# Performance work log

Measured on AMD Instinct MI355X. Metric: run time of the kernel, lower is better.

The kernel has to match this reference:

```python
import jax, jax.numpy as jnp
import numpy as np

N = 20000      # nodes
E = 320000     # edges (before self-loops)
IN = 128       # in_features
H = 8          # heads
C = 120        # out channels per head
SLOPE = 0.2    # LeakyReLU negative slope (PyG default)


def setup_inputs() -> dict:
    key = jax.random.key(0)
    k = jax.random.split(key, 8)
    x = jax.random.normal(k[0], (N, IN), jnp.float32)
    edge_index = jax.random.randint(k[1], (2, E), 0, N)  # [2,E], row0=src, row1=dst
    W = jax.random.normal(k[2], (IN, H * C), jnp.float32) / np.sqrt(IN)
    att_src = jax.random.normal(k[3], (H, C), jnp.float32) * 0.1
    att_dst = jax.random.normal(k[4], (H, C), jnp.float32) * 0.1
    bias = jnp.zeros((H * C,), jnp.float32)
    fc_w = jax.random.normal(k[5], (H * C, 2), jnp.float32) / np.sqrt(H * C)
    fc_b = jnp.zeros((2,), jnp.float32)
    return dict(x=x, edge_index=edge_index, W=W, att_src=att_src,
                att_dst=att_dst, bias=bias, fc_w=fc_w, fc_b=fc_b)


def reference(x, edge_index, W, att_src, att_dst, bias, fc_w, fc_b):
    n = x.shape[0]
    # add self loops (GATConv default add_self_loops=True)
    loops = jnp.arange(n, dtype=edge_index.dtype)
    ei = jnp.concatenate([edge_index, jnp.stack([loops, loops])], axis=1)
    src, dst = ei[0], ei[1]
    # per-head linear projection: [n, H, C]
    xp = (x @ W).reshape(n, H, C)
    # per-node attention logits
    a_s = jnp.einsum('nhc,hc->nh', xp, att_src)  # [n,H]
    a_d = jnp.einsum('nhc,hc->nh', xp, att_dst)  # [n,H]
    # edge-wise logits + LeakyReLU: [Etot,H]
    e = jax.nn.leaky_relu(a_s[src] + a_d[dst], SLOPE)
    # segment softmax over incoming edges of each destination node
    emax = jax.lax.stop_gradient(jax.ops.segment_max(e, dst, num_segments=n))
    ee = jnp.exp(e - emax[dst])
    denom = jax.ops.segment_sum(ee, dst, num_segments=n)
    alpha = ee / denom[dst]                      # [Etot,H]
    # scatter-aggregate weighted messages: [n,H,C]
    out = jax.ops.segment_sum(alpha[:, :, None] * xp[src], dst, num_segments=n)
    out = out.reshape(n, H * C) + bias           # concat heads + bias
    return out @ fc_w + fc_b                     # final Linear -> [n,2]
```

## Files before the change

kernel.cpp:

```cpp
#include <hip/hip_runtime.h>

#define NN    20000
#define EDGES 320000
#define HH    8
#define CC    120
#define HC    960
#define SLOPE 0.2f
#define BUCKET 64
#define NB    64
#define CH    (EDGES / NB)
#define NPAIR (NN / 2)


__global__ __launch_bounds__(256) void prep_kernel(const float* __restrict__ W,
                                                   const float* __restrict__ att_src,
                                                   const float* __restrict__ att_dst,
                                                   const float* __restrict__ bias,
                                                   const float* __restrict__ fc_w,
                                                   const float* __restrict__ fc_b,
                                                   const int* __restrict__ ei,
                                                   float* __restrict__ U,
                                                   float* __restrict__ cbias,
                                                   unsigned* __restrict__ hist,
                                                   unsigned* __restrict__ rank) {
  __shared__ unsigned hsh[NPAIR];
  int t = threadIdx.x, b = blockIdx.x;
  int l = t & 63;
  if (b < 256) {
    int p = b * 4 + (t >> 6);
    int k = p >> 3, h = p & 7;
    const float* wrow = W + (size_t)k * HC + h * CC;
    const float* asv  = att_src + h * CC;
    const float* adv  = att_dst + h * CC;
    const float2* fv  = (const float2*)fc_w + h * CC;
    bool tail = (l < CC - 64);
    float w0 = wrow[l],            w1 = tail ? wrow[64 + l] : 0.f;
    float s0 = asv[l],             s1 = tail ? asv[64 + l] : 0.f;
    float d0 = adv[l],             d1 = tail ? adv[64 + l] : 0.f;
    float2 f0 = fv[l];
    float2 f1 = tail ? fv[64 + l] : make_float2(0.f, 0.f);
    float a_s = w0 * s0 + w1 * s1;
    float a_d = w0 * d0 + w1 * d1;
    float z0  = w0 * f0.x + w1 * f1.x;
    float z1  = w0 * f0.y + w1 * f1.y;
#pragma unroll
    for (int m = 1; m < 64; m <<= 1) {
      a_s += __shfl_xor(a_s, m);
      a_d += __shfl_xor(a_d, m);
      z0  += __shfl_xor(z0, m);
      z1  += __shfl_xor(z1, m);
    }
    if (l == 0) {
      float* u = U + k * 32 + 4 * h;
      u[0] = a_s; u[1] = z0; u[2] = z1; u[3] = a_d;
    }
  } else if (b == 256) {
    if (t < 128) {
      int j = t >> 6;
      float acc = 0.f;
      for (int m = l; m < HC; m += 64) acc = fmaf(bias[m], fc_w[m * 2 + j], acc);
#pragma unroll
      for (int m = 1; m < 64; m <<= 1) acc += __shfl_xor(acc, m);
      if (l == 0) cbias[j] = acc + fc_b[j];
    }
  } else {
    int c = b - 257;
    for (int i = t; i < NPAIR; i += 256) hsh[i] = 0u;
    __syncthreads();
    const int* dsts = ei + EDGES + c * CH;
    unsigned* rnk = rank + c * CH;
    for (int i = t; i < CH; i += 256) {
      int d = dsts[i];
      unsigned old = atomicAdd(&hsh[d >> 1], (d & 1) ? (1u << 16) : 1u);
      rnk[i] = (d & 1) ? (old >> 16) : (old & 0xFFFFu);
    }
    __syncthreads();
    unsigned* hrow = hist + (size_t)c * NPAIR;
    for (int i = t; i < NPAIR; i += 256) hrow[i] = hsh[i];
  }
}

__global__ __launch_bounds__(256) void scan_kernel(const unsigned* __restrict__ hist,
                                                   unsigned* __restrict__ base,
                                                   unsigned* __restrict__ deg) {
  int j = blockIdx.x * 256 + threadIdx.x;
  if (j >= NPAIR) return;
  unsigned sA = 0, sB = 0;
#pragma unroll 8
  for (int c = 0; c < NB; ++c) {
    unsigned v = hist[(size_t)c * NPAIR + j];
    base[(size_t)c * NPAIR + j] = sA | (sB << 16);
    sA += v & 0xFFFFu;
    sB += v >> 16;
  }
  deg[2 * j]     = sA;
  deg[2 * j + 1] = sB;
}

#define XSTR 132
__global__ __launch_bounds__(128) void projplace_kernel(const float* __restrict__ x,
                                                        const float* __restrict__ U,
                                                        const int* __restrict__ ei,
                                                        const unsigned* __restrict__ base,
                                                        const unsigned* __restrict__ rank,
                                                        unsigned* __restrict__ list,
                                                        float* __restrict__ P) {
  int t = threadIdx.x;
  int b = blockIdx.x;

  if (b >= 625) {
    int e0 = (b - 625) * 256 + t;
#pragma unroll
    for (int j = 0; j < 2; ++j) {
      int e = e0 + j * 128;
      int d = ei[EDGES + e];
      unsigned r = rank[e];
      unsigned c = (unsigned)e / (unsigned)CH;
      unsigned packed = base[(size_t)c * NPAIR + (d >> 1)];
      unsigned bs = (d & 1) ? (packed >> 16) : (packed & 0xFFFFu);
      list[(size_t)d * BUCKET + bs + r] = (unsigned)ei[e];
    }
    return;
  }

  __shared__ float xs[32 * XSTR];
  __shared__ float Us[128 * 32];
  int n0 = b * 32;
  const float4* xg = (const float4*)(x + (size_t)n0 * 128);
  const float4* U4 = (const float4*)U;
  float4 xv[8], uv[8];
#pragma unroll
  for (int j = 0; j < 8; ++j) xv[j] = xg[t + j * 128];
#pragma unroll
  for (int j = 0; j < 8; ++j) uv[j] = U4[t + j * 128];
#pragma unroll
  for (int j = 0; j < 8; ++j) {
    int i = t + j * 128;
    *(float4*)(xs + (i >> 5) * XSTR + (i & 31) * 4) = xv[j];
    ((float4*)Us)[i] = uv[j];
  }
  __syncthreads();

  int rq = t >> 3, cq = t & 7;
  float a00 = 0.f, a01 = 0.f, a02 = 0.f, a03 = 0.f;
  float a10 = 0.f, a11 = 0.f, a12 = 0.f, a13 = 0.f;
  const float* xr0 = xs + rq * XSTR;
  const float* xr1 = xs + (rq + 16) * XSTR;
#pragma unroll 4
  for (int k4 = 0; k4 < 32; ++k4) {
    float4 xa = *(const float4*)(xr0 + k4 * 4);
    float4 xb = *(const float4*)(xr1 + k4 * 4);
    float4 u0 = *(const float4*)(Us + (k4 * 4 + 0) * 32 + 4 * cq);
    float4 u1 = *(const float4*)(Us + (k4 * 4 + 1) * 32 + 4 * cq);
    float4 u2 = *(const float4*)(Us + (k4 * 4 + 2) * 32 + 4 * cq);
    float4 u3 = *(const float4*)(Us + (k4 * 4 + 3) * 32 + 4 * cq);
    a00 = fmaf(xa.x, u0.x, a00); a01 = fmaf(xa.x, u0.y, a01);
    a02 = fmaf(xa.x, u0.z, a02); a03 = fmaf(xa.x, u0.w, a03);
    a10 = fmaf(xb.x, u0.x, a10); a11 = fmaf(xb.x, u0.y, a11);
    a12 = fmaf(xb.x, u0.z, a12); a13 = fmaf(xb.x, u0.w, a13);
    a00 = fmaf(xa.y, u1.x, a00); a01 = fmaf(xa.y, u1.y, a01);
    a02 = fmaf(xa.y, u1.z, a02); a03 = fmaf(xa.y, u1.w, a03);
    a10 = fmaf(xb.y, u1.x, a10); a11 = fmaf(xb.y, u1.y, a11);
    a12 = fmaf(xb.y, u1.z, a12); a13 = fmaf(xb.y, u1.w, a13);
    a00 = fmaf(xa.z, u2.x, a00); a01 = fmaf(xa.z, u2.y, a01);
    a02 = fmaf(xa.z, u2.z, a02); a03 = fmaf(xa.z, u2.w, a03);
    a10 = fmaf(xb.z, u2.x, a10); a11 = fmaf(xb.z, u2.y, a11);
    a12 = fmaf(xb.z, u2.z, a12); a13 = fmaf(xb.z, u2.w, a13);
    a00 = fmaf(xa.w, u3.x, a00); a01 = fmaf(xa.w, u3.y, a01);
    a02 = fmaf(xa.w, u3.z, a02); a03 = fmaf(xa.w, u3.w, a03);
    a10 = fmaf(xb.w, u3.x, a10); a11 = fmaf(xb.w, u3.y, a11);
    a12 = fmaf(xb.w, u3.z, a12); a13 = fmaf(xb.w, u3.w, a13);
  }
  *(float4*)(P + (size_t)(n0 + rq) * 32 + 4 * cq) =
      make_float4(a00, a01, a02, a03);
  *(float4*)(P + (size_t)(n0 + rq + 16) * 32 + 4 * cq) =
      make_float4(a10, a11, a12, a13);
}

__global__ __launch_bounds__(256) void gather_kernel(const unsigned* __restrict__ deg_,
                                                     const unsigned* __restrict__ list,
                                                     const float* __restrict__ P,
                                                     const float* __restrict__ cbias,
                                                     float* __restrict__ out) {
  int t = threadIdx.x;
  int wave = t >> 6;
  int lane = t & 63;
  int h = lane & 7;
  int o = lane >> 3;
  int dst = blockIdx.x * 4 + wave;

  const float* pd = P + (size_t)dst * 32;
  float4 pd4 = *(const float4*)(pd + 4 * h);
  float ad = pd4.w;
  unsigned deg = deg_[dst];
  unsigned rv = list[(size_t)dst * BUCKET + lane];

  float accd = 0.f, acc0 = 0.f, acc1 = 0.f;
  if (o == 0) {
    float v = pd4.x + ad;
    v = (v > 0.f) ? v : SLOPE * v;
    float ex = __expf(v);
    accd = ex;
    acc0 = ex * pd4.y;
    acc1 = ex * pd4.z;
  }

  unsigned e0 = o, e1 = o + 8, e2 = o + 16, e3 = o + 24;
  unsigned s0 = __shfl(rv, (int)e0);
  unsigned s1 = __shfl(rv, (int)e1);
  unsigned s2 = __shfl(rv, (int)e2);
  unsigned s3 = __shfl(rv, (int)e3);
  bool m0 = e0 < deg, m1 = e1 < deg, m2 = e2 < deg, m3 = e3 < deg;
  unsigned a0 = m0 ? s0 : (unsigned)dst;
  unsigned a1 = m1 ? s1 : (unsigned)dst;
  unsigned a2 = m2 ? s2 : (unsigned)dst;
  unsigned a3 = m3 ? s3 : (unsigned)dst;
  float4 q0 = *(const float4*)(P + (size_t)a0 * 32 + 4 * h);
  float4 q1 = *(const float4*)(P + (size_t)a1 * 32 + 4 * h);
  float4 q2 = *(const float4*)(P + (size_t)a2 * 32 + 4 * h);
  float4 q3 = *(const float4*)(P + (size_t)a3 * 32 + 4 * h);
  if (m0) {
    float v = q0.x + ad; v = (v > 0.f) ? v : SLOPE * v;
    float ex = __expf(v);
    accd += ex; acc0 = fmaf(ex, q0.y, acc0); acc1 = fmaf(ex, q0.z, acc1);
  }
  if (m1) {
    float v = q1.x + ad; v = (v > 0.f) ? v : SLOPE * v;
    float ex = __expf(v);
    accd += ex; acc0 = fmaf(ex, q1.y, acc0); acc1 = fmaf(ex, q1.z, acc1);
  }
  if (m2) {
    float v = q2.x + ad; v = (v > 0.f) ? v : SLOPE * v;
    float ex = __expf(v);
    accd += ex; acc0 = fmaf(ex, q2.y, acc0); acc1 = fmaf(ex, q2.z, acc1);
  }
  if (m3) {
    float v = q3.x + ad; v = (v > 0.f) ? v : SLOPE * v;
    float ex = __expf(v);
    accd += ex; acc0 = fmaf(ex, q3.y, acc0); acc1 = fmaf(ex, q3.z, acc1);
  }
  if (deg > 32u) {
    unsigned iters = (deg - 32u + 7u) >> 3;
    unsigned e = 32u + (unsigned)o;
    for (unsigned i = 0; i < iters; ++i, e += 8u) {
      unsigned src = __shfl(rv, (int)e);
      if (e < deg) {
        float4 q = *(const float4*)(P + (size_t)src * 32 + 4 * h);
        float v = q.x + ad; v = (v > 0.f) ? v : SLOPE * v;
        float ex = __expf(v);
        accd += ex; acc0 = fmaf(ex, q.y, acc0); acc1 = fmaf(ex, q.z, acc1);
      }
    }
  }
  float accd_tot = accd + __shfl_xor(accd, 8);
  accd_tot += __shfl_xor(accd_tot, 16);
  accd_tot += __shfl_xor(accd_tot, 32);
  float rcp = 1.0f / accd_tot;
  float r0 = acc0 * rcp;
  float r1 = acc1 * rcp;
#pragma unroll
  for (int m = 1; m < 64; m <<= 1) {
    r0 += __shfl_xor(r0, m);
    r1 += __shfl_xor(r1, m);
  }
  if (lane == 0) {
    ((float2*)out)[dst] = make_float2(cbias[0] + r0, cbias[1] + r1);
  }
}

extern "C" void kernel_launch(void* const* d_in, const int* in_sizes, int n_in,
                              void* d_out, int out_size, void* d_ws, size_t ws_size,
                              hipStream_t stream) {
  const float* x       = (const float*)d_in[0];
  const int*   ei      = (const int*)d_in[1];
  const float* W       = (const float*)d_in[2];
  const float* att_src = (const float*)d_in[3];
  const float* att_dst = (const float*)d_in[4];
  const float* bias    = (const float*)d_in[5];
  const float* fc_w    = (const float*)d_in[6];
  const float* fc_b    = (const float*)d_in[7];
  float* out = (float*)d_out;

  float*    U     = (float*)d_ws;
  float*    cbias = U + 4096;
  float*    P     = U + 8192;
  unsigned* deg   = (unsigned*)(P + (size_t)NN * 32);
  unsigned* list  = deg + NN;
  unsigned* hist  = list + (size_t)NN * BUCKET;
  unsigned* base  = hist + (size_t)NB * NPAIR;
  unsigned* rank  = base + (size_t)NB * NPAIR;

  prep_kernel<<<321, 256, 0, stream>>>(W, att_src, att_dst, bias, fc_w, fc_b,
                                       ei, U, cbias, hist, rank);
  scan_kernel<<<40, 256, 0, stream>>>(hist, base, deg);
  projplace_kernel<<<1875, 128, 0, stream>>>(x, U, ei, base, rank, list, P);
  gather_kernel<<<NN / 4, 256, 0, stream>>>(deg, list, P, cbias, out);
}
```

Baseline: 38.78 us.

## Pack histogram into 8-bit counters, double chunk count, read x directly

The per-chunk destination histogram now packs four 8-bit counters per word with 128 edge chunks instead of two 16-bit counters with 64 chunks. This halves the shared histogram size and shrinks the scan to 5000 columns, and ranks are stored as bytes to cut traffic. Histogram blocks are reordered to come first in the prep launch, the projection kernel reads x rows straight from global memory instead of staging them in LDS, and the gather kernel skips the second pair of neighbour loads when degree is at most 16. The byte counters assume no destination ever exceeds 255 entries, which holds only because the bucket is 64 slots.

```diff
diff --git a/kernel.cpp b/kernel.cpp
--- a/kernel.cpp
+++ b/kernel.cpp
@@ -7,9 +7,9 @@
 #define HC    960
 #define SLOPE 0.2f
 #define BUCKET 64
-#define NB    64
+#define NB    128
 #define CH    (EDGES / NB)
-#define NPAIR (NN / 2)
+#define NQ    (NN / 4)
 
 
 __global__ __launch_bounds__(256) void prep_kernel(const float* __restrict__ W,
@@ -22,12 +22,26 @@
                                                    float* __restrict__ U,
                                                    float* __restrict__ cbias,
                                                    unsigned* __restrict__ hist,
-                                                   unsigned* __restrict__ rank) {
-  __shared__ unsigned hsh[NPAIR];
+                                                   unsigned char* __restrict__ rank) {
+  __shared__ unsigned hsh[NQ];
   int t = threadIdx.x, b = blockIdx.x;
   int l = t & 63;
-  if (b < 256) {
-    int p = b * 4 + (t >> 6);
+  if (b < NB) {
+    for (int i = t; i < NQ; i += 256) hsh[i] = 0u;
+    __syncthreads();
+    const int* dsts = ei + EDGES + b * CH;
+    unsigned char* rnk = rank + b * CH;
+    for (int i = t; i < CH; i += 256) {
+      int d = dsts[i];
+      unsigned sh = (d & 3) * 8;
+      unsigned old = atomicAdd(&hsh[d >> 2], 1u << sh);
+      rnk[i] = (unsigned char)(old >> sh);
+    }
+    __syncthreads();
+    unsigned* hrow = hist + (size_t)b * NQ;
+    for (int i = t; i < NQ; i += 256) hrow[i] = hsh[i];
+  } else if (b < 384) {
+    int p = (b - 128) * 4 + (t >> 6);
     int k = p >> 3, h = p & 7;
     const float* wrow = W + (size_t)k * HC + h * CC;
     const float* asv  = att_src + h * CC;
@@ -54,55 +68,39 @@
       float* u = U + k * 32 + 4 * h;
       u[0] = a_s; u[1] = z0; u[2] = z1; u[3] = a_d;
     }
-  } else if (b == 256) {
-    if (t < 128) {
-      int j = t >> 6;
-      float acc = 0.f;
-      for (int m = l; m < HC; m += 64) acc = fmaf(bias[m], fc_w[m * 2 + j], acc);
-#pragma unroll
-      for (int m = 1; m < 64; m <<= 1) acc += __shfl_xor(acc, m);
-      if (l == 0) cbias[j] = acc + fc_b[j];
-    }
-  } else {
-    int c = b - 257;
-    for (int i = t; i < NPAIR; i += 256) hsh[i] = 0u;
-    __syncthreads();
-    const int* dsts = ei + EDGES + c * CH;
-    unsigned* rnk = rank + c * CH;
-    for (int i = t; i < CH; i += 256) {
-      int d = dsts[i];
-      unsigned old = atomicAdd(&hsh[d >> 1], (d & 1) ? (1u << 16) : 1u);
-      rnk[i] = (d & 1) ? (old >> 16) : (old & 0xFFFFu);
-    }
-    __syncthreads();
-    unsigned* hrow = hist + (size_t)c * NPAIR;
-    for (int i = t; i < NPAIR; i += 256) hrow[i] = hsh[i];
+  } else if (t < 128) {
+    int j = t >> 6;
+    float acc = 0.f;
+    for (int m = l; m < HC; m += 64) acc = fmaf(bias[m], fc_w[m * 2 + j], acc);
+#pragma unroll
+    for (int m = 1; m < 64; m <<= 1) acc += __shfl_xor(acc, m);
+    if (l == 0) cbias[j] = acc + fc_b[j];
   }
 }
 
 __global__ __launch_bounds__(256) void scan_kernel(const unsigned* __restrict__ hist,
                                                    unsigned* __restrict__ base,
-                                                   unsigned* __restrict__ deg) {
+                                                   uint4* __restrict__ deg4) {
   int j = blockIdx.x * 256 + threadIdx.x;
-  if (j >= NPAIR) return;
-  unsigned sA = 0, sB = 0;
+  if (j >= NQ) return;
+  unsigned s0 = 0, s1 = 0, s2 = 0, s3 = 0;
 #pragma unroll 8
   for (int c = 0; c < NB; ++c) {
-    unsigned v = hist[(size_t)c * NPAIR + j];
-    base[(size_t)c * NPAIR + j] = sA | (sB << 16);
-    sA += v & 0xFFFFu;
-    sB += v >> 16;
-  }
-  deg[2 * j]     = sA;
-  deg[2 * j + 1] = sB;
-}
-
-#define XSTR 132
+    unsigned v = hist[(size_t)c * NQ + j];
+    base[(size_t)c * NQ + j] = s0 | (s1 << 8) | (s2 << 16) | (s3 << 24);
+    s0 += v & 0xFFu;
+    s1 += (v >> 8) & 0xFFu;
+    s2 += (v >> 16) & 0xFFu;
+    s3 += (v >> 24) & 0xFFu;
+  }
+  deg4[j] = make_uint4(s0, s1, s2, s3);
+}
+
 __global__ __launch_bounds__(128) void projplace_kernel(const float* __restrict__ x,
                                                         const float* __restrict__ U,
                                                         const int* __restrict__ ei,
                                                         const unsigned* __restrict__ base,
-                                                        const unsigned* __restrict__ rank,
+                                                        const unsigned char* __restrict__ rank,
                                                         unsigned* __restrict__ list,
                                                         float* __restrict__ P) {
   int t = threadIdx.x;
@@ -116,40 +114,29 @@
       int d = ei[EDGES + e];
       unsigned r = rank[e];
       unsigned c = (unsigned)e / (unsigned)CH;
-      unsigned packed = base[(size_t)c * NPAIR + (d >> 1)];
-      unsigned bs = (d & 1) ? (packed >> 16) : (packed & 0xFFFFu);
+      unsigned packed = base[(size_t)c * NQ + (d >> 2)];
+      unsigned bs = (packed >> ((d & 3) * 8)) & 0xFFu;
       list[(size_t)d * BUCKET + bs + r] = (unsigned)ei[e];
     }
     return;
   }
 
-  __shared__ float xs[32 * XSTR];
   __shared__ float Us[128 * 32];
   int n0 = b * 32;
-  const float4* xg = (const float4*)(x + (size_t)n0 * 128);
   const float4* U4 = (const float4*)U;
-  float4 xv[8], uv[8];
-#pragma unroll
-  for (int j = 0; j < 8; ++j) xv[j] = xg[t + j * 128];
-#pragma unroll
-  for (int j = 0; j < 8; ++j) uv[j] = U4[t + j * 128];
-#pragma unroll
-  for (int j = 0; j < 8; ++j) {
-    int i = t + j * 128;
-    *(float4*)(xs + (i >> 5) * XSTR + (i & 31) * 4) = xv[j];
-    ((float4*)Us)[i] = uv[j];
-  }
+#pragma unroll
+  for (int j = 0; j < 8; ++j) ((float4*)Us)[t + j * 128] = U4[t + j * 128];
   __syncthreads();
 
   int rq = t >> 3, cq = t & 7;
+  const float4* xr0 = (const float4*)(x + (size_t)(n0 + rq) * 128);
+  const float4* xr1 = (const float4*)(x + (size_t)(n0 + rq + 16) * 128);
   float a00 = 0.f, a01 = 0.f, a02 = 0.f, a03 = 0.f;
   float a10 = 0.f, a11 = 0.f, a12 = 0.f, a13 = 0.f;
-  const float* xr0 = xs + rq * XSTR;
-  const float* xr1 = xs + (rq + 16) * XSTR;
 #pragma unroll 4
   for (int k4 = 0; k4 < 32; ++k4) {
-    float4 xa = *(const float4*)(xr0 + k4 * 4);
-    float4 xb = *(const float4*)(xr1 + k4 * 4);
+    float4 xa = xr0[k4];
+    float4 xb = xr1[k4];
     float4 u0 = *(const float4*)(Us + (k4 * 4 + 0) * 32 + 4 * cq);
     float4 u1 = *(const float4*)(Us + (k4 * 4 + 1) * 32 + 4 * cq);
     float4 u2 = *(const float4*)(Us + (k4 * 4 + 2) * 32 + 4 * cq);
@@ -205,39 +192,45 @@
     acc1 = ex * pd4.z;
   }
 
-  unsigned e0 = o, e1 = o + 8, e2 = o + 16, e3 = o + 24;
-  unsigned s0 = __shfl(rv, (int)e0);
-  unsigned s1 = __shfl(rv, (int)e1);
-  unsigned s2 = __shfl(rv, (int)e2);
-  unsigned s3 = __shfl(rv, (int)e3);
-  bool m0 = e0 < deg, m1 = e1 < deg, m2 = e2 < deg, m3 = e3 < deg;
-  unsigned a0 = m0 ? s0 : (unsigned)dst;
-  unsigned a1 = m1 ? s1 : (unsigned)dst;
-  unsigned a2 = m2 ? s2 : (unsigned)dst;
-  unsigned a3 = m3 ? s3 : (unsigned)dst;
-  float4 q0 = *(const float4*)(P + (size_t)a0 * 32 + 4 * h);
-  float4 q1 = *(const float4*)(P + (size_t)a1 * 32 + 4 * h);
-  float4 q2 = *(const float4*)(P + (size_t)a2 * 32 + 4 * h);
-  float4 q3 = *(const float4*)(P + (size_t)a3 * 32 + 4 * h);
-  if (m0) {
-    float v = q0.x + ad; v = (v > 0.f) ? v : SLOPE * v;
-    float ex = __expf(v);
-    accd += ex; acc0 = fmaf(ex, q0.y, acc0); acc1 = fmaf(ex, q0.z, acc1);
-  }
-  if (m1) {
-    float v = q1.x + ad; v = (v > 0.f) ? v : SLOPE * v;
-    float ex = __expf(v);
-    accd += ex; acc0 = fmaf(ex, q1.y, acc0); acc1 = fmaf(ex, q1.z, acc1);
-  }
-  if (m2) {
-    float v = q2.x + ad; v = (v > 0.f) ? v : SLOPE * v;
-    float ex = __expf(v);
-    accd += ex; acc0 = fmaf(ex, q2.y, acc0); acc1 = fmaf(ex, q2.z, acc1);
-  }
-  if (m3) {
-    float v = q3.x + ad; v = (v > 0.f) ? v : SLOPE * v;
-    float ex = __expf(v);
-    accd += ex; acc0 = fmaf(ex, q3.y, acc0); acc1 = fmaf(ex, q3.z, acc1);
+  {
+    unsigned e0 = o, e1 = o + 8;
+    unsigned s0 = __shfl(rv, (int)e0);
+    unsigned s1 = __shfl(rv, (int)e1);
+    bool m0 = e0 < deg, m1 = e1 < deg;
+    unsigned a0 = m0 ? s0 : (unsigned)dst;
+    unsigned a1 = m1 ? s1 : (unsigned)dst;
+    float4 q0 = *(const float4*)(P + (size_t)a0 * 32 + 4 * h);
+    float4 q1 = *(const float4*)(P + (size_t)a1 * 32 + 4 * h);
+    if (m0) {
+      float v = q0.x + ad; v = (v > 0.f) ? v : SLOPE * v;
+      float ex = __expf(v);
+      accd += ex; acc0 = fmaf(ex, q0.y, acc0); acc1 = fmaf(ex, q0.z, acc1);
+    }
+    if (m1) {
+      float v = q1.x + ad; v = (v > 0.f) ? v : SLOPE * v;
+      float ex = __expf(v);
+      accd += ex; acc0 = fmaf(ex, q1.y, acc0); acc1 = fmaf(ex, q1.z, acc1);
+    }
+  }
+  if (deg > 16u) {
+    unsigned e2 = o + 16, e3 = o + 24;
+    unsigned s2 = __shfl(rv, (int)e2);
+    unsigned s3 = __shfl(rv, (int)e3);
+    bool m2 = e2 < deg, m3 = e3 < deg;
+    unsigned a2 = m2 ? s2 : (unsigned)dst;
+    unsigned a3 = m3 ? s3 : (unsigned)dst;
+    float4 q2 = *(const float4*)(P + (size_t)a2 * 32 + 4 * h);
+    float4 q3 = *(const float4*)(P + (size_t)a3 * 32 + 4 * h);
+    if (m2) {
+      float v = q2.x + ad; v = (v > 0.f) ? v : SLOPE * v;
+      float ex = __expf(v);
+      accd += ex; acc0 = fmaf(ex, q2.y, acc0); acc1 = fmaf(ex, q2.z, acc1);
+    }
+    if (m3) {
+      float v = q3.x + ad; v = (v > 0.f) ? v : SLOPE * v;
+      float ex = __expf(v);
+      accd += ex; acc0 = fmaf(ex, q3.y, acc0); acc1 = fmaf(ex, q3.z, acc1);
+    }
   }
   if (deg > 32u) {
     unsigned iters = (deg - 32u + 7u) >> 3;
@@ -287,12 +280,12 @@
   unsigned* deg   = (unsigned*)(P + (size_t)NN * 32);
   unsigned* list  = deg + NN;
   unsigned* hist  = list + (size_t)NN * BUCKET;
-  unsigned* base  = hist + (size_t)NB * NPAIR;
-  unsigned* rank  = base + (size_t)NB * NPAIR;
-
-  prep_kernel<<<321, 256, 0, stream>>>(W, att_src, att_dst, bias, fc_w, fc_b,
+  unsigned* base  = hist + (size_t)NB * NQ;
+  unsigned char* rank = (unsigned char*)(base + (size_t)NB * NQ);
+
+  prep_kernel<<<385, 256, 0, stream>>>(W, att_src, att_dst, bias, fc_w, fc_b,
                                        ei, U, cbias, hist, rank);
-  scan_kernel<<<40, 256, 0, stream>>>(hist, base, deg);
+  scan_kernel<<<20, 256, 0, stream>>>(hist, base, (uint4*)deg);
   projplace_kernel<<<1875, 128, 0, stream>>>(x, U, ei, base, rank, list, P);
   gather_kernel<<<NN / 4, 256, 0, stream>>>(deg, list, P, cbias, out);
 }
```

Measured after the change: 45.80 us. 18.1% more time.
